# Optimization experiments

Measured on AMD Instinct MI355X. Metric: run time of the kernel, lower is better.

Reference implementation:

```python
import jax, jax.numpy as jnp
import numpy as np

C = 256
HEAD = 4
HEAD_DIM = C // HEAD
B, N, M = 8, 4096, 4096
EPS = 1e-5


def _conv1x1(x, w, b):
    # x: [B, Cin, N], w: [Cout, Cin], b: [Cout]
    return jnp.einsum('oc,bcn->bon', w, x) + b[None, :, None]


def setup_inputs() -> dict:
    key = jax.random.key(0)
    ks = jax.random.split(key, 16)
    s = 0.02
    inp = {
        'motion1': jax.random.normal(ks[0], (B, C, N), jnp.float32),
        'motion2': jax.random.normal(ks[1], (B, C, M), jnp.float32),
        'wq': jax.random.normal(ks[2], (C, C), jnp.float32) * s,
        'bq': jnp.zeros((C,), jnp.float32),
        'wk': jax.random.normal(ks[3], (C, C), jnp.float32) * s,
        'bk': jnp.zeros((C,), jnp.float32),
        'wv': jax.random.normal(ks[4], (C, C), jnp.float32) * s,
        'bv': jnp.zeros((C,), jnp.float32),
        'wm': jax.random.normal(ks[5], (C, C), jnp.float32) * s,
        'bm': jnp.zeros((C,), jnp.float32),
        'w1': jax.random.normal(ks[6], (2 * C, 2 * C), jnp.float32) * s,
        'b1': jnp.zeros((2 * C,), jnp.float32),
        'gamma': jnp.ones((2 * C,), jnp.float32),
        'beta': jnp.zeros((2 * C,), jnp.float32),
        'w2': jax.random.normal(ks[7], (C, 2 * C), jnp.float32) * s,
        'b2': jnp.zeros((C,), jnp.float32),
    }
    return inp


def reference(motion1, motion2, wq, bq, wk, bk, wv, bv, wm, bm,
              w1, b1, gamma, beta, w2, b2):
    bsz = motion1.shape[0]
    # QKV via 1x1 conv (pointwise linear over channels), split heads
    q = _conv1x1(motion1, wq, bq).reshape(bsz, HEAD, HEAD_DIM, -1)  # [B,H,D,N]
    k = _conv1x1(motion2, wk, bk).reshape(bsz, HEAD, HEAD_DIM, -1)  # [B,H,D,M]
    v = _conv1x1(motion2, wv, bv).reshape(bsz, HEAD, HEAD_DIM, -1)  # [B,H,D,M]
    # full cross-attention score [B,H,N,M]
    score = jax.nn.softmax(
        jnp.einsum('bhdn,bhdm->bhnm', q, k) / (HEAD_DIM ** 0.5), axis=-1)
    add_value = jnp.einsum('bhnm,bhdm->bhdn', score, v).reshape(bsz, HEAD * HEAD_DIM, -1)
    add_value = _conv1x1(add_value, wm, bm)
    # cat_filter: conv1x1 -> BatchNorm1d (training-mode batch stats) -> ReLU -> conv1x1
    h = _conv1x1(jnp.concatenate([motion1, add_value], axis=1), w1, b1)  # [B,2C,N]
    mean = jnp.mean(h, axis=(0, 2), keepdims=True)
    var = jnp.var(h, axis=(0, 2), keepdims=True)
    h = (h - mean) * jax.lax.rsqrt(var + EPS)
    h = h * gamma[None, :, None] + beta[None, :, None]
    h = jax.nn.relu(h)
    return motion1 + _conv1x1(h, w2, b2)
```

## Files before the change

kernel.cpp:

```cpp
#include <hip/hip_runtime.h>
#include <stdint.h>

#define B_  8
#define C_  256
#define H_  4
#define D_  64
#define N_  4096
#define C2_ 512
#define NT_ (B_*N_)

typedef __attribute__((ext_vector_type(8))) short short8;
typedef __attribute__((ext_vector_type(4))) short short4_t;
typedef __attribute__((ext_vector_type(4))) float f32x4;

__device__ __forceinline__ short f2bf(float f) {
  union { float f; unsigned u; } v; v.f = f;
  unsigned r = v.u + 0x7fffu + ((v.u >> 16) & 1u);
  return (short)(r >> 16);
}
__device__ __forceinline__ float bfraw2f(unsigned hi_bits) {
  union { unsigned u; float f; } v; v.u = hi_bits;
  return v.f;
}
__device__ __forceinline__ unsigned fbits(float f) {
  union { float f; unsigned u; } v; v.f = f; return v.u;
}

#if __has_builtin(__builtin_amdgcn_exp2f)
#define EXP2(x) __builtin_amdgcn_exp2f(x)
#else
#define EXP2(x) exp2f(x)
#endif

#define GLOAD16(g, l) __builtin_amdgcn_global_load_lds( \
    (const __attribute__((address_space(1))) void*)(g), \
    (__attribute__((address_space(3))) void*)(l), 16, 0, 0)

__global__ __launch_bounds__(256) void prep_wcat(
    const float* __restrict__ w1, const float* __restrict__ wm,
    const float* __restrict__ b1, const float* __restrict__ bm,
    short* __restrict__ wcat, float* __restrict__ beff, float* __restrict__ stats)
{
  int i = blockIdx.x, j = threadIdx.x;
  wcat[(size_t)i*512 + j] = f2bf(w1[(size_t)i*512 + j]);
  float acc = 0.f;
  for (int c = 0; c < 256; ++c)
    acc += w1[(size_t)i*512 + 256 + c] * wm[(size_t)c*256 + j];
  wcat[(size_t)i*512 + 256 + j] = f2bf(acc);
  if (j == 0) {
    float a = b1[i];
    for (int c = 0; c < 256; ++c) a += w1[(size_t)i*512 + 256 + c] * bm[c];
    beff[i] = a;
  }
  if (blockIdx.x < 4) stats[blockIdx.x*256 + j] = 0.f;
}

__global__ void cvt_bf16(const float* __restrict__ src, short* __restrict__ dst, int n) {
  int i = blockIdx.x*256 + threadIdx.x;
  if (i < n) dst[i] = f2bf(src[i]);
}

__global__ __launch_bounds__(256) void transpose_cvt(
    const float* __restrict__ m1, const float* __restrict__ m2,
    short* __restrict__ xt1, short* __restrict__ mt2)
{
  __shared__ float tile[32][33];
  int z = blockIdx.z;
  int b = z >> 1, which = z & 1;
  const float* src = which ? m2 : m1;
  short* dst = which ? mt2 : xt1;
  int ldd = which ? 256 : 512;
  int c0 = blockIdx.y*32, n0 = blockIdx.x*32;
  int tx = threadIdx.x & 31, ty = threadIdx.x >> 5;
  for (int r = 0; r < 4; ++r) {
    int c = c0 + ty + r*8;
    tile[ty + r*8][tx] = src[((size_t)b*256 + c)*4096 + n0 + tx];
  }
  __syncthreads();
  for (int r = 0; r < 4; ++r) {
    int n = n0 + ty + r*8;
    dst[((size_t)b*4096 + n)*ldd + c0 + tx] = f2bf(tile[tx][ty + r*8]);
  }
}

template<int MODE>
__global__ __launch_bounds__(256) void gemm_bt(
    const short* __restrict__ A, int lda,
    const short* __restrict__ Bm, int ldb,
    const float* __restrict__ bias, float scale, int Kc,
    void* __restrict__ OutP, const float* __restrict__ resid)
{
  __shared__ __align__(16) short As[128*64];
  __shared__ __align__(16) short Bs[128*64];
  const int tid  = threadIdx.x;
  const int wave = tid >> 6, lane = tid & 63;
  const int it = blockIdx.y, jt = blockIdx.x, bz = blockIdx.z;
  const int i0 = it*128, j0 = jt*128;
  const short* Bb = Bm + (size_t)bz * 4096 * ldb;
  const int wi = wave >> 1, wj = wave & 1;
  const int l15 = lane & 15, lg = lane >> 4;

  f32x4 acc[4][4] = {};

  for (int k0 = 0; k0 < Kc; k0 += 64) {
    __syncthreads();
    for (int s = 0; s < 4; ++s) {
      int flat = s*256 + tid;
      int row = flat >> 3, l8 = flat & 7;
      GLOAD16(A  + (size_t)(i0 + row)*lda + k0 + l8*8, &As[(s*256 + wave*64)*8]);
      GLOAD16(Bb + (size_t)(j0 + row)*ldb + k0 + l8*8, &Bs[(s*256 + wave*64)*8]);
    }
    __syncthreads();
    for (int ks = 0; ks < 2; ++ks) {
      short8 af[4], bf[4];
      for (int mt = 0; mt < 4; ++mt)
        af[mt] = *(const short8*)&As[(wi*64 + mt*16 + l15)*64 + ks*32 + lg*8];
      for (int nt = 0; nt < 4; ++nt)
        bf[nt] = *(const short8*)&Bs[(wj*64 + nt*16 + l15)*64 + ks*32 + lg*8];
      for (int mt = 0; mt < 4; ++mt)
        for (int nt = 0; nt < 4; ++nt)
          acc[mt][nt] = __builtin_amdgcn_mfma_f32_16x16x32_bf16(af[mt], bf[nt], acc[mt][nt], 0, 0, 0);
    }
  }

  for (int mt = 0; mt < 4; ++mt)
    for (int nt = 0; nt < 4; ++nt)
      for (int r = 0; r < 4; ++r) {
        int i = i0 + wi*64 + mt*16 + lg*4 + r;
        int j = j0 + wj*64 + nt*16 + l15;
        float v = acc[mt][nt][r] + bias[i];
        if (MODE == 0) {
          v *= scale;
          short* out = (short*)OutP + (size_t)bz*C_*N_;
          out[((size_t)((i >> 6)*4096 + j))*64 + (i & 63)] = f2bf(v);
        } else if (MODE == 1) {
          short* out = (short*)OutP + (size_t)bz*C_*N_;
          out[(size_t)i*4096 + j] = f2bf(v);
        } else if (MODE == 2) {
          ((short*)OutP)[(size_t)j*512 + i] = f2bf(v);
        } else {
          size_t oi = ((size_t)(j >> 12)*256 + i)*4096 + (j & 4095);
          ((float*)OutP)[oi] = v + resid[oi];
        }
      }
}

__global__ __launch_bounds__(256, 2) void flash_attn(
    const short* __restrict__ qb, const short* __restrict__ kb,
    const short* __restrict__ vb, short* __restrict__ xt1)
{
  __shared__ __align__(16) short K_lds[64*64];
  __shared__ __align__(16) short V_lds[64*64];
  const int tid = threadIdx.x, wave = tid >> 6, lane = tid & 63;
  const int l15 = lane & 15, lg = lane >> 4;
  const int bh = blockIdx.y, qt = blockIdx.x;
  const int b = bh >> 2, h = bh & 3;
  const short* qbase = qb + (size_t)bh*4096*64;
  const short* kbase = kb + (size_t)bh*4096*64;
  const short* vbase = vb + ((size_t)b*256 + h*64)*4096;
  const int q0 = qt*256 + wave*64;

  int c0 = tid, c1 = 256 + tid;
  int row0 = c0 >> 3, x0 = (c0 & 7) ^ (row0 & 7);
  int row1 = c1 >> 3, x1 = (c1 & 7) ^ (row1 & 7);
  const short* kg0 = kbase + row0*64 + x0*8;
  const short* kg1 = kbase + row1*64 + x1*8;
  const short* vg0 = vbase + (size_t)row0*4096 + x0*8;
  const short* vg1 = vbase + (size_t)row1*4096 + x1*8;

  short8 qf[4][2];
  for (int rt = 0; rt < 4; ++rt) {
    int q = q0 + rt*16 + l15;
    for (int hf = 0; hf < 2; ++hf)
      qf[rt][hf] = *(const short8*)(qbase + (size_t)q*64 + hf*32 + lg*8);
  }

  f32x4 o[4][4] = {};
  float rs[4] = {0.f, 0.f, 0.f, 0.f};

  for (int m0 = 0; m0 < 4096; m0 += 64) {
    __syncthreads();
    GLOAD16(kg0 + (size_t)m0*64, &K_lds[(0*256 + wave*64)*8]);
    GLOAD16(kg1 + (size_t)m0*64, &K_lds[(1*256 + wave*64)*8]);
    GLOAD16(vg0 + m0,            &V_lds[(0*256 + wave*64)*8]);
    GLOAD16(vg1 + m0,            &V_lds[(1*256 + wave*64)*8]);
    __syncthreads();

    short8 kf[4][2];
    for (int ct = 0; ct < 4; ++ct) {
      int row = ct*16 + l15;
      for (int hf = 0; hf < 2; ++hf) {
        int s = (hf*4 + lg) ^ (row & 7);
        kf[ct][hf] = *(const short8*)&K_lds[row*64 + s*8];
      }
    }
    short8 vf[2][4];
    for (int p = 0; p < 2; ++p)
      for (int dt = 0; dt < 4; ++dt) {
        int d = dt*16 + l15;
        int mc1 = p*4 + (lg >> 1), mc2 = mc1 + 2;
        int off1 = (d*8 + (mc1 ^ (d & 7)))*8 + (lg & 1)*4;
        int off2 = (d*8 + (mc2 ^ (d & 7)))*8 + (lg & 1)*4;
        union { short8 v; short4_t h[2]; } u;
        u.h[0] = *(const short4_t*)&V_lds[off1];
        u.h[1] = *(const short4_t*)&V_lds[off2];
        vf[p][dt] = u.v;
      }

    for (int rt = 0; rt < 4; ++rt) {
      f32x4 sc[4];
      for (int ct = 0; ct < 4; ++ct) {
        f32x4 s = {0.f, 0.f, 0.f, 0.f};
        s = __builtin_amdgcn_mfma_f32_16x16x32_bf16(kf[ct][0], qf[rt][0], s, 0, 0, 0);
        s = __builtin_amdgcn_mfma_f32_16x16x32_bf16(kf[ct][1], qf[rt][1], s, 0, 0, 0);
        sc[ct] = s;
      }
      for (int p = 0; p < 2; ++p) {
        union { short8 v; unsigned u[4]; } pf;
        for (int idx = 0; idx < 2; ++idx) {
          f32x4 sv = sc[2*p + idx];
          float e0 = EXP2(sv[0]), e1 = EXP2(sv[1]);
          float e2 = EXP2(sv[2]), e3 = EXP2(sv[3]);
          rs[rt] += (e0 + e1) + (e2 + e3);
          pf.u[idx*2 + 0] = __builtin_amdgcn_perm(fbits(e1) + 0x8000u, fbits(e0) + 0x8000u, 0x07060302u);
          pf.u[idx*2 + 1] = __builtin_amdgcn_perm(fbits(e3) + 0x8000u, fbits(e2) + 0x8000u, 0x07060302u);
        }
        for (int dt = 0; dt < 4; ++dt)
          o[rt][dt] = __builtin_amdgcn_mfma_f32_16x16x32_bf16(pf.v, vf[p][dt], o[rt][dt], 0, 0, 0);
      }
    }
  }

  for (int rt = 0; rt < 4; ++rt) {
    float v = rs[rt];
    v += __shfl_xor(v, 16);
    v += __shfl_xor(v, 32);
    rs[rt] = 1.0f / v;
  }
  for (int rt = 0; rt < 4; ++rt) {
    float invq[4];
    for (int r = 0; r < 4; ++r) invq[r] = __shfl(rs[rt], lg*4 + r);
    for (int dt = 0; dt < 4; ++dt)
      for (int r = 0; r < 4; ++r) {
        int q = q0 + rt*16 + lg*4 + r;
        int d = dt*16 + l15;
        float val = o[rt][dt][r] * invq[r];
        xt1[((size_t)b*4096 + q)*512 + 256 + h*64 + d] = f2bf(val);
      }
  }
}

__global__ __launch_bounds__(256) void bn_stats(const short* __restrict__ ht,
                                                float* __restrict__ stats)
{
  int p = blockIdx.x, t = threadIdx.x;
  int c0 = t*2;
  float s0=0.f, s1=0.f, q0=0.f, q1=0.f;
  for (int r = 0; r < 256; ++r) {
    size_t row = (size_t)p*256 + r;
    unsigned v = *(const unsigned*)&ht[row*512 + c0];
    float x0 = bfraw2f(v << 16);
    float x1 = bfraw2f(v & 0xffff0000u);
    s0 += x0; q0 += x0*x0; s1 += x1; q1 += x1*x1;
  }
  atomicAdd(&stats[c0],       s0);
  atomicAdd(&stats[c0+1],     s1);
  atomicAdd(&stats[512+c0],   q0);
  atomicAdd(&stats[512+c0+1], q1);
}

__global__ void bn_final(const float* __restrict__ stats,
                         const float* __restrict__ gamma, const float* __restrict__ beta,
                         float* __restrict__ ss)
{
  int c = blockIdx.x*256 + threadIdx.x;
  if (c >= 512) return;
  float mean = stats[c] * (1.f/32768.f);
  float var  = stats[512+c] * (1.f/32768.f) - mean*mean;
  float sc = gamma[c] * rsqrtf(var + 1e-5f);
  ss[c] = sc;
  ss[512+c] = beta[c] - mean*sc;
}

__global__ __launch_bounds__(256) void relu_affine(short* __restrict__ ht,
                                                   const float* __restrict__ ss)
{
  size_t idx = (size_t)blockIdx.x*256 + threadIdx.x;
  unsigned v = ((unsigned*)ht)[idx];
  int c0 = (int)((idx*2) & 511);
  float x0 = bfraw2f(v << 16);
  float x1 = bfraw2f(v & 0xffff0000u);
  float y0 = x0 * ss[c0]   + ss[512+c0];
  float y1 = x1 * ss[c0+1] + ss[512+c0+1];
  y0 = y0 > 0.f ? y0 : 0.f;
  y1 = y1 > 0.f ? y1 : 0.f;
  unsigned p0 = (unsigned)(unsigned short)f2bf(y0);
  unsigned p1 = (unsigned)(unsigned short)f2bf(y1);
  ((unsigned*)ht)[idx] = p0 | (p1 << 16);
}

extern "C" void kernel_launch(void* const* d_in, const int* in_sizes, int n_in,
                              void* d_out, int out_size, void* d_ws, size_t ws_size,
                              hipStream_t stream)
{
  const float* m1    = (const float*)d_in[0];
  const float* m2    = (const float*)d_in[1];
  const float* wq    = (const float*)d_in[2];
  const float* bq    = (const float*)d_in[3];
  const float* wk    = (const float*)d_in[4];
  const float* bk    = (const float*)d_in[5];
  const float* wv    = (const float*)d_in[6];
  const float* bv    = (const float*)d_in[7];
  const float* wm    = (const float*)d_in[8];
  const float* bm    = (const float*)d_in[9];
  const float* w1    = (const float*)d_in[10];
  const float* b1    = (const float*)d_in[11];
  const float* gamma = (const float*)d_in[12];
  const float* beta  = (const float*)d_in[13];
  const float* w2    = (const float*)d_in[14];
  const float* b2    = (const float*)d_in[15];

  char* ws = (char*)d_ws;
  size_t o = 0;
  short* XT1 = (short*)(ws + o); o += (size_t)NT_*512*2;
  short* MT2 = (short*)(ws + o); o += (size_t)NT_*256*2;
  size_t qoff = o;
  short* QB  = (short*)(ws + o); o += (size_t)NT_*256*2;
  short* KB  = (short*)(ws + o); o += (size_t)NT_*256*2;
  short* VB  = (short*)(ws + o); o += (size_t)NT_*256*2;
  short* HT  = (short*)(ws + qoff);
  short* WQ  = (short*)(ws + o); o += 256*256*2;
  short* WK  = (short*)(ws + o); o += 256*256*2;
  short* WV  = (short*)(ws + o); o += 256*256*2;
  short* W2B = (short*)(ws + o); o += 256*512*2;
  short* WCAT= (short*)(ws + o); o += 512*512*2;
  float* BEFF= (float*)(ws + o); o += 512*4;
  float* STATS=(float*)(ws + o); o += 1024*4;
  float* SS  = (float*)(ws + o); o += 1024*4;
  if (ws_size < o) return;

  prep_wcat<<<512, 256, 0, stream>>>(w1, wm, b1, bm, WCAT, BEFF, STATS);
  cvt_bf16<<<256, 256, 0, stream>>>(wq, WQ, 256*256);
  cvt_bf16<<<256, 256, 0, stream>>>(wk, WK, 256*256);
  cvt_bf16<<<256, 256, 0, stream>>>(wv, WV, 256*256);
  cvt_bf16<<<512, 256, 0, stream>>>(w2, W2B, 256*512);
  transpose_cvt<<<dim3(128, 8, 16), 256, 0, stream>>>(m1, m2, XT1, MT2);

  gemm_bt<0><<<dim3(32, 2, 8), 256, 0, stream>>>(WQ, 256, XT1, 512, bq, 0.18033688f, 256, QB, nullptr);
  gemm_bt<0><<<dim3(32, 2, 8), 256, 0, stream>>>(WK, 256, MT2, 256, bk, 1.0f,        256, KB, nullptr);
  gemm_bt<1><<<dim3(32, 2, 8), 256, 0, stream>>>(WV, 256, MT2, 256, bv, 1.0f,        256, VB, nullptr);

  flash_attn<<<dim3(16, 32), 256, 0, stream>>>(QB, KB, VB, XT1);

  gemm_bt<2><<<dim3(256, 4, 1), 256, 0, stream>>>(WCAT, 512, XT1, 512, BEFF, 1.0f, 512, HT, nullptr);
  bn_stats<<<128, 256, 0, stream>>>(HT, STATS);
  bn_final<<<2, 256, 0, stream>>>(STATS, gamma, beta, SS);
  relu_affine<<<32768, 256, 0, stream>>>(HT, SS);
  gemm_bt<3><<<dim3(256, 2, 1), 256, 0, stream>>>(W2B, 512, HT, 512, b2, 1.0f, 512, d_out, m1);
}
```

Before: 449.6 us.

## Double-buffer K/V tiles in flash attention and merge weight conversion launches

The flash attention loop now keeps two LDS buffers for K and V and issues the async global-to-LDS loads for the next tile before computing on the current one. This removes one barrier per iteration and lets memory traffic overlap the MFMA and exp work. Swizzled LDS offsets are precomputed outside the loop, the row-sum accumulates as a vector, and bf16 packing now truncates instead of rounding. The four weight conversion kernels are merged into one launch. LDS use per block doubles, which may limit occupancy, and the last iteration issues a redundant wrap-around load.

After: 433.0 us. -3.7%, faster.

```diff
diff --git a/kernel.cpp b/kernel.cpp
--- a/kernel.cpp
+++ b/kernel.cpp
@@ -55,9 +55,17 @@
   if (blockIdx.x < 4) stats[blockIdx.x*256 + j] = 0.f;
 }
 
-__global__ void cvt_bf16(const float* __restrict__ src, short* __restrict__ dst, int n) {
+__global__ __launch_bounds__(256) void cvt4_bf16(
+    const float* __restrict__ s0, const float* __restrict__ s1,
+    const float* __restrict__ s2, const float* __restrict__ s3,
+    short* __restrict__ d0, short* __restrict__ d1,
+    short* __restrict__ d2, short* __restrict__ d3)
+{
   int i = blockIdx.x*256 + threadIdx.x;
-  if (i < n) dst[i] = f2bf(src[i]);
+  if (i < 65536)        d0[i]          = f2bf(s0[i]);
+  else if (i < 131072)  d1[i - 65536]  = f2bf(s1[i - 65536]);
+  else if (i < 196608)  d2[i - 131072] = f2bf(s2[i - 131072]);
+  else                  d3[i - 196608] = f2bf(s3[i - 196608]);
 }
 
 __global__ __launch_bounds__(256) void transpose_cvt(
@@ -149,8 +157,8 @@
     const short* __restrict__ qb, const short* __restrict__ kb,
     const short* __restrict__ vb, short* __restrict__ xt1)
 {
-  __shared__ __align__(16) short K_lds[64*64];
-  __shared__ __align__(16) short V_lds[64*64];
+  __shared__ __align__(16) short K_lds[2][64*64];
+  __shared__ __align__(16) short V_lds[2][64*64];
   const int tid = threadIdx.x, wave = tid >> 6, lane = tid & 63;
   const int l15 = lane & 15, lg = lane >> 4;
   const int bh = blockIdx.y, qt = blockIdx.x;
@@ -167,6 +175,23 @@
   const short* kg1 = kbase + row1*64 + x1*8;
   const short* vg0 = vbase + (size_t)row0*4096 + x0*8;
   const short* vg1 = vbase + (size_t)row1*4096 + x1*8;
+  const unsigned ldsA = (unsigned)((wave*64)*8);
+  const unsigned ldsB = (unsigned)((256 + wave*64)*8);
+
+  unsigned kOff[4][2];
+  for (int ct = 0; ct < 4; ++ct) {
+    int row = ct*16 + l15;
+    for (int hf = 0; hf < 2; ++hf)
+      kOff[ct][hf] = (unsigned)(row*64 + (((hf*4 + lg) ^ (row & 7))*8));
+  }
+  unsigned vOff[2][4][2];
+  for (int p = 0; p < 2; ++p)
+    for (int dt = 0; dt < 4; ++dt) {
+      int d = dt*16 + l15;
+      int mc1 = p*4 + (lg >> 1), mc2 = mc1 + 2;
+      vOff[p][dt][0] = (unsigned)((d*8 + (mc1 ^ (d & 7)))*8 + (lg & 1)*4);
+      vOff[p][dt][1] = (unsigned)((d*8 + (mc2 ^ (d & 7)))*8 + (lg & 1)*4);
+    }
 
   short8 qf[4][2];
   for (int rt = 0; rt < 4; ++rt) {
@@ -176,34 +201,35 @@
   }
 
   f32x4 o[4][4] = {};
-  float rs[4] = {0.f, 0.f, 0.f, 0.f};
-
-  for (int m0 = 0; m0 < 4096; m0 += 64) {
+  f32x4 rs4[4] = {};
+
+  GLOAD16(kg0, &K_lds[0][ldsA]);
+  GLOAD16(kg1, &K_lds[0][ldsB]);
+  GLOAD16(vg0, &V_lds[0][ldsA]);
+  GLOAD16(vg1, &V_lds[0][ldsB]);
+
+  for (int itv = 0; itv < 64; ++itv) {
     __syncthreads();
-    GLOAD16(kg0 + (size_t)m0*64, &K_lds[(0*256 + wave*64)*8]);
-    GLOAD16(kg1 + (size_t)m0*64, &K_lds[(1*256 + wave*64)*8]);
-    GLOAD16(vg0 + m0,            &V_lds[(0*256 + wave*64)*8]);
-    GLOAD16(vg1 + m0,            &V_lds[(1*256 + wave*64)*8]);
-    __syncthreads();
+    const int cur = itv & 1, nxt = cur ^ 1;
+    const size_t mN = (size_t)(((itv + 1) & 63) * 64);
+    GLOAD16(kg0 + mN*64, &K_lds[nxt][ldsA]);
+    GLOAD16(kg1 + mN*64, &K_lds[nxt][ldsB]);
+    GLOAD16(vg0 + mN,    &V_lds[nxt][ldsA]);
+    GLOAD16(vg1 + mN,    &V_lds[nxt][ldsB]);
+
+    const short* Kb = &K_lds[cur][0];
+    const short* Vb = &V_lds[cur][0];
 
     short8 kf[4][2];
-    for (int ct = 0; ct < 4; ++ct) {
-      int row = ct*16 + l15;
-      for (int hf = 0; hf < 2; ++hf) {
-        int s = (hf*4 + lg) ^ (row & 7);
-        kf[ct][hf] = *(const short8*)&K_lds[row*64 + s*8];
-      }
-    }
+    for (int ct = 0; ct < 4; ++ct)
+      for (int hf = 0; hf < 2; ++hf)
+        kf[ct][hf] = *(const short8*)(Kb + kOff[ct][hf]);
     short8 vf[2][4];
     for (int p = 0; p < 2; ++p)
       for (int dt = 0; dt < 4; ++dt) {
-        int d = dt*16 + l15;
-        int mc1 = p*4 + (lg >> 1), mc2 = mc1 + 2;
-        int off1 = (d*8 + (mc1 ^ (d & 7)))*8 + (lg & 1)*4;
-        int off2 = (d*8 + (mc2 ^ (d & 7)))*8 + (lg & 1)*4;
         union { short8 v; short4_t h[2]; } u;
-        u.h[0] = *(const short4_t*)&V_lds[off1];
-        u.h[1] = *(const short4_t*)&V_lds[off2];
+        u.h[0] = *(const short4_t*)(Vb + vOff[p][dt][0]);
+        u.h[1] = *(const short4_t*)(Vb + vOff[p][dt][1]);
         vf[p][dt] = u.v;
       }
 
@@ -219,11 +245,12 @@
         union { short8 v; unsigned u[4]; } pf;
         for (int idx = 0; idx < 2; ++idx) {
           f32x4 sv = sc[2*p + idx];
-          float e0 = EXP2(sv[0]), e1 = EXP2(sv[1]);
-          float e2 = EXP2(sv[2]), e3 = EXP2(sv[3]);
-          rs[rt] += (e0 + e1) + (e2 + e3);
-          pf.u[idx*2 + 0] = __builtin_amdgcn_perm(fbits(e1) + 0x8000u, fbits(e0) + 0x8000u, 0x07060302u);
-          pf.u[idx*2 + 1] = __builtin_amdgcn_perm(fbits(e3) + 0x8000u, fbits(e2) + 0x8000u, 0x07060302u);
+          f32x4 ev;
+          ev[0] = EXP2(sv[0]); ev[1] = EXP2(sv[1]);
+          ev[2] = EXP2(sv[2]); ev[3] = EXP2(sv[3]);
+          rs4[rt] += ev;
+          pf.u[idx*2 + 0] = __builtin_amdgcn_perm(fbits(ev[1]), fbits(ev[0]), 0x07060302u);
+          pf.u[idx*2 + 1] = __builtin_amdgcn_perm(fbits(ev[3]), fbits(ev[2]), 0x07060302u);
         }
         for (int dt = 0; dt < 4; ++dt)
           o[rt][dt] = __builtin_amdgcn_mfma_f32_16x16x32_bf16(pf.v, vf[p][dt], o[rt][dt], 0, 0, 0);
@@ -231,15 +258,16 @@
     }
   }
 
+  float rsI[4];
   for (int rt = 0; rt < 4; ++rt) {
-    float v = rs[rt];
+    float v = (rs4[rt][0] + rs4[rt][1]) + (rs4[rt][2] + rs4[rt][3]);
     v += __shfl_xor(v, 16);
     v += __shfl_xor(v, 32);
-    rs[rt] = 1.0f / v;
+    rsI[rt] = 1.0f / v;
   }
   for (int rt = 0; rt < 4; ++rt) {
     float invq[4];
-    for (int r = 0; r < 4; ++r) invq[r] = __shfl(rs[rt], lg*4 + r);
+    for (int r = 0; r < 4; ++r) invq[r] = __shfl(rsI[rt], lg*4 + r);
     for (int dt = 0; dt < 4; ++dt)
       for (int r = 0; r < 4; ++r) {
         int q = q0 + rt*16 + lg*4 + r;
@@ -340,10 +368,7 @@
   if (ws_size < o) return;
 
   prep_wcat<<<512, 256, 0, stream>>>(w1, wm, b1, bm, WCAT, BEFF, STATS);
-  cvt_bf16<<<256, 256, 0, stream>>>(wq, WQ, 256*256);
-  cvt_bf16<<<256, 256, 0, stream>>>(wk, WK, 256*256);
-  cvt_bf16<<<256, 256, 0, stream>>>(wv, WV, 256*256);
-  cvt_bf16<<<512, 256, 0, stream>>>(w2, W2B, 256*512);
+  cvt4_bf16<<<1280, 256, 0, stream>>>(wq, wk, wv, w2, WQ, WK, WV, W2B);
   transpose_cvt<<<dim3(128, 8, 16), 256, 0, stream>>>(m1, m2, XT1, MT2);
 
   gemm_bt<0><<<dim3(32, 2, 8), 256, 0, stream>>>(WQ, 256, XT1, 512, bq, 0.18033688f, 256, QB, nullptr);
```
